# Optimization experiments

Hardware: AMD Instinct MI355X
Metric: run time of the kernel (lower is better)

Reference implementation:

```python
import jax, jax.numpy as jnp
import numpy as np

NEG_SLOPE = 0.2


def _attn_layer(x, src, dst, W, a, n_nodes):
    # x: (N, Cin), W: (Cout, Cin) torch Linear convention, a: (2*Cout,)
    h = x @ W.T                                  # (N, Cout)
    H = h.shape[-1]
    # cat([x_i, x_j]) @ a  ==  h[dst] @ a[:H] + h[src] @ a[H:]
    s_i = h @ a[:H]                              # (N,)
    s_j = h @ a[H:]                              # (N,)
    score = s_i[dst] + s_j[src]                  # (E,)
    alpha = jax.nn.leaky_relu(score, NEG_SLOPE)
    # segment softmax over destination nodes
    amax = jax.ops.segment_max(alpha, dst, num_segments=n_nodes)
    amax = jnp.where(jnp.isfinite(amax), amax, 0.0)
    ex = jnp.exp(alpha - amax[dst])
    denom = jax.ops.segment_sum(ex, dst, num_segments=n_nodes)
    alpha = ex / denom[dst]                      # (E,)
    msg = h[src] * alpha[:, None]                # (E, Cout)
    sums = jax.ops.segment_sum(msg, dst, num_segments=n_nodes)
    cnt = jax.ops.segment_sum(jnp.ones_like(alpha), dst, num_segments=n_nodes)
    return sums / jnp.maximum(cnt, 1.0)[:, None]  # mean aggregation


def setup_inputs() -> dict:
    key = jax.random.key(0)
    ks = jax.random.split(key, 8)
    B, N, C, H, E = 16, 2048, 256, 256, 262144
    NT = B * N
    temporal_features = jax.random.normal(ks[0], (B, N, C), dtype=jnp.float32)
    edge_index = jax.random.randint(ks[1], (2, E), 0, NT, dtype=jnp.int64)
    sc = 1.0 / np.sqrt(C)
    W1 = jax.random.normal(ks[2], (H, C), dtype=jnp.float32) * sc
    a1 = jax.random.normal(ks[3], (2 * H,), dtype=jnp.float32) * sc
    W2 = jax.random.normal(ks[4], (H, H), dtype=jnp.float32) * sc
    a2 = jax.random.normal(ks[5], (2 * H,), dtype=jnp.float32) * sc
    W3 = jax.random.normal(ks[6], (H, H), dtype=jnp.float32) * sc
    a3 = jax.random.normal(ks[7], (2 * H,), dtype=jnp.float32) * sc
    return {"temporal_features": temporal_features, "edge_index": edge_index,
            "W1": W1, "a1": a1, "W2": W2, "a2": a2, "W3": W3, "a3": a3}


def reference(temporal_features, edge_index, W1, a1, W2, a2, W3, a3):
    B, N, C = temporal_features.shape
    n_nodes = B * N
    src, dst = edge_index[0], edge_index[1]  # x_j = x[src], x_i = x[dst]
    x = temporal_features.reshape(n_nodes, C)
    for W, a in ((W1, a1), (W2, a2), (W3, a3)):
        x = _attn_layer(x, src, dst, W, a, n_nodes)
        x = jax.nn.elu(x)
    return x.reshape(B, N, -1)
```

## Files before the change

### kernel.cpp

```cpp
#include <hip/hip_runtime.h>
#include <math.h>
#include <stdint.h>


typedef float f32x4 __attribute__((ext_vector_type(4)));
typedef _Float16 f16x8 __attribute__((ext_vector_type(8)));
typedef _Float16 f16x4 __attribute__((ext_vector_type(4)));


__global__ __launch_bounds__(256) void convert_all(const float* __restrict__ x0,
                                                   _Float16* __restrict__ Xh, int nx,
                                                   const float* __restrict__ W0,
                                                   const float* __restrict__ W1,
                                                   const float* __restrict__ W2,
                                                   _Float16* __restrict__ Wh)
{
    const int i = (blockIdx.x * 256 + threadIdx.x) * 8;
    const float* src;
    _Float16* dstp;
    int off;
    if (i < nx) { src = x0; dstp = Xh; off = i; }
    else {
        const int j = i - nx;
        src = (j < 65536) ? W0 : ((j < 131072) ? W1 : W2);
        off = j & 65535;
        dstp = Wh + (j - off);
    }
    float4 a = *(const float4*)&src[off];
    float4 b = *(const float4*)&src[off + 4];
    f16x8 o = {(_Float16)a.x, (_Float16)a.y, (_Float16)a.z, (_Float16)a.w,
               (_Float16)b.x, (_Float16)b.y, (_Float16)b.z, (_Float16)b.w};
    *(f16x8*)&dstp[off] = o;
}


#define SWZ(row, byte) ((byte) ^ (((row) & 7) << 4))

__global__ __launch_bounds__(512) void gemm_f16(const _Float16* __restrict__ X,
                                                const _Float16* __restrict__ Wh,
                                                const float* __restrict__ avec,
                                                _Float16* __restrict__ Hout,
                                                float* __restrict__ si,
                                                float* __restrict__ sj)
{
    __shared__ __align__(16) unsigned char smem[98304];
    float (*Es)[260] = (float (*)[260])smem;

    const int tid  = threadIdx.x;
    const int lane = tid & 63;
    const int w    = tid >> 6;
    const int wr   = w >> 2;
    const int wc   = w & 3;
    const int ln   = lane & 15;
    const int kq   = lane >> 4;
    const int m0   = blockIdx.x * 128;

    const int xr = tid >> 2;
    const int xc = tid & 3;
    const int wrow = tid >> 1;
    const int wcb  = (tid & 1) * 64;

    const _Float16* Xg = X  + (size_t)(m0 + xr) * 256 + xc * 16;
    const _Float16* Wg = Wh + (size_t)wrow * 256 + wcb / 2;
    const int xs0 = SWZ(xr, xr * 128 + xc * 32);
    const int xs1 = SWZ(xr, xr * 128 + xc * 32 + 16);
    const int wl0 = 16384 + SWZ(wrow, wrow * 128 + wcb + 0);
    const int wl1 = 16384 + SWZ(wrow, wrow * 128 + wcb + 16);
    const int wl2 = 16384 + SWZ(wrow, wrow * 128 + wcb + 32);
    const int wl3 = 16384 + SWZ(wrow, wrow * 128 + wcb + 48);

    f32x4 acc[4][4] = {};

    f16x8 x0 = *(const f16x8*)&Xg[0];
    f16x8 x1 = *(const f16x8*)&Xg[8];
    f16x8 w0 = *(const f16x8*)&Wg[0];
    f16x8 w1 = *(const f16x8*)&Wg[8];
    f16x8 w2 = *(const f16x8*)&Wg[16];
    f16x8 w3 = *(const f16x8*)&Wg[24];
    *(f16x8*)(smem + xs0) = x0;  *(f16x8*)(smem + xs1) = x1;
    *(f16x8*)(smem + wl0) = w0;  *(f16x8*)(smem + wl1) = w1;
    *(f16x8*)(smem + wl2) = w2;  *(f16x8*)(smem + wl3) = w3;
    __syncthreads();

#pragma unroll
    for (int t = 0; t < 4; ++t) {
        const int cb = (t & 1) * 49152;
        const int nb = ((t & 1) ^ 1) * 49152;
        if (t < 3) {
            const int k0 = (t + 1) * 64;
            x0 = *(const f16x8*)&Xg[k0];
            x1 = *(const f16x8*)&Xg[k0 + 8];
            w0 = *(const f16x8*)&Wg[k0];
            w1 = *(const f16x8*)&Wg[k0 + 8];
            w2 = *(const f16x8*)&Wg[k0 + 16];
            w3 = *(const f16x8*)&Wg[k0 + 24];
        }
#pragma unroll
        for (int kk = 0; kk < 2; ++kk) {
            f16x8 af[4], bf[4];
#pragma unroll
            for (int i = 0; i < 4; ++i) {
                const int row = wr * 64 + i * 16 + ln;
                af[i] = *(const f16x8*)(smem + cb + SWZ(row, row * 128 + kk * 64 + kq * 16));
            }
#pragma unroll
            for (int j = 0; j < 4; ++j) {
                const int row = wc * 64 + j * 16 + ln;
                bf[j] = *(const f16x8*)(smem + cb + 16384 + SWZ(row, row * 128 + kk * 64 + kq * 16));
            }
#pragma unroll
            for (int i = 0; i < 4; ++i)
#pragma unroll
                for (int j = 0; j < 4; ++j)
                    acc[i][j] = __builtin_amdgcn_mfma_f32_16x16x32_f16(af[i], bf[j], acc[i][j], 0, 0, 0);
        }
        if (t < 3) {
            *(f16x8*)(smem + nb + xs0) = x0;  *(f16x8*)(smem + nb + xs1) = x1;
            *(f16x8*)(smem + nb + wl0) = w0;  *(f16x8*)(smem + nb + wl1) = w1;
            *(f16x8*)(smem + nb + wl2) = w2;  *(f16x8*)(smem + nb + wl3) = w3;
        }
        __syncthreads();
    }

    const int er = tid >> 5;
    const int ec = tid & 31;
    for (int g = 0; g < 8; ++g) {
        if (wr == (g >> 2)) {
            const int i = g & 3;
#pragma unroll
            for (int j = 0; j < 4; ++j) {
                const int col = wc * 64 + j * 16 + ln;
#pragma unroll
                for (int q = 0; q < 4; ++q)
                    Es[kq * 4 + q][col] = acc[i][j][q];
            }
        }
        __syncthreads();
        const int grow = m0 + g * 16 + er;
        const int c0 = ec * 8;
        f32x4 v0 = *(const f32x4*)&Es[er][c0];
        f32x4 v1 = *(const f32x4*)&Es[er][c0 + 4];
        f16x8 ho = {(_Float16)v0[0], (_Float16)v0[1], (_Float16)v0[2], (_Float16)v0[3],
                    (_Float16)v1[0], (_Float16)v1[1], (_Float16)v1[2], (_Float16)v1[3]};
        *(f16x8*)&Hout[(size_t)grow * 256 + c0] = ho;

        f32x4 al0 = *(const f32x4*)&avec[c0];
        f32x4 al1 = *(const f32x4*)&avec[c0 + 4];
        f32x4 ah0 = *(const f32x4*)&avec[256 + c0];
        f32x4 ah1 = *(const f32x4*)&avec[256 + c0 + 4];
        float d0 = v0[0]*al0[0] + v0[1]*al0[1] + v0[2]*al0[2] + v0[3]*al0[3]
                 + v1[0]*al1[0] + v1[1]*al1[1] + v1[2]*al1[2] + v1[3]*al1[3];
        float d1 = v0[0]*ah0[0] + v0[1]*ah0[1] + v0[2]*ah0[2] + v0[3]*ah0[3]
                 + v1[0]*ah1[0] + v1[1]*ah1[1] + v1[2]*ah1[2] + v1[3]*ah1[3];
#pragma unroll
        for (int d = 16; d; d >>= 1) {
            d0 += __shfl_xor(d0, d);
            d1 += __shfl_xor(d1, d);
        }
        if (ec == 0) { si[grow] = d0; sj[grow] = d1; }
        __syncthreads();
    }
}


__global__ void zero_int(int* p, int n)
{
    int i = blockIdx.x * blockDim.x + threadIdx.x;
    if (i < n) p[i] = 0;
}

__global__ void hist_kernel(const int* __restrict__ dst, int* __restrict__ cnt, int E)
{
    int e = blockIdx.x * blockDim.x + threadIdx.x;
    if (e < E) atomicAdd(&cnt[dst[e]], 1);
}

__global__ __launch_bounds__(1024) void scan_part(const int* __restrict__ cnt,
                                                  int* __restrict__ off,
                                                  int* __restrict__ bsum)
{
    __shared__ int buf[1024];
    const int tid = threadIdx.x;
    const int g = blockIdx.x * 1024 + tid;
    int v = cnt[g];
    buf[tid] = v;
    __syncthreads();
#pragma unroll
    for (int d = 1; d < 1024; d <<= 1) {
        int t = (tid >= d) ? buf[tid - d] : 0;
        __syncthreads();
        buf[tid] += t;
        __syncthreads();
    }
    off[g] = buf[tid] - v;
    if (tid == 1023) bsum[blockIdx.x] = buf[1023];
}

__global__ void scan_bsum(int* bsum, int nb)
{
    __shared__ int b[64];
    const int tid = threadIdx.x;
    b[tid] = (tid < nb) ? bsum[tid] : 0;
    __syncthreads();
    if (tid == 0) {
        int a = 0;
        for (int i = 0; i < nb; ++i) { int t = b[i]; b[i] = a; a += t; }
    }
    __syncthreads();
    if (tid < nb) bsum[tid] = b[tid];
}

__global__ __launch_bounds__(1024) void scan_add(const int* __restrict__ bsum,
                                                 int* __restrict__ off,
                                                 int* __restrict__ cursor,
                                                 int NT, int E)
{
    const int tid = threadIdx.x;
    const int g = blockIdx.x * 1024 + tid;
    int v = off[g] + bsum[blockIdx.x];
    off[g] = v;
    cursor[g] = v;
    if (g == 0) off[NT] = E;
}

__global__ void scatter_kernel(const int* __restrict__ src,
                               const int* __restrict__ dst,
                               int* __restrict__ cursor,
                               int* __restrict__ ssrc, int E)
{
    int e = blockIdx.x * blockDim.x + threadIdx.x;
    if (e < E) {
        int p = atomicAdd(&cursor[dst[e]], 1);
        ssrc[p] = src[e];
    }
}


__device__ __forceinline__ float bcast_f(float x, int l)
{
    return __uint_as_float(__builtin_amdgcn_readlane(__float_as_uint(x), l));
}

template <int F16OUT>
__global__ __launch_bounds__(256) void aggregate(const _Float16* __restrict__ Hh,
                                                 const float* __restrict__ si,
                                                 const float* __restrict__ sj,
                                                 const int* __restrict__ off,
                                                 const int* __restrict__ ssrc,
                                                 void* __restrict__ outv,
                                                 int n_nodes)
{
    const int v = (blockIdx.x * 256 + threadIdx.x) >> 6;
    const int lane = threadIdx.x & 63;
    if (v >= n_nodes) return;

    const int e0 = off[v], e1 = off[v + 1];
    const int deg = e1 - e0;
    f32x4 acc = {0.f, 0.f, 0.f, 0.f};

    if (deg > 0 && deg <= 64) {
        const float siv = si[v];
        const int idx = e0 + lane;
        const bool on = idx < e1;
        int s = 0;
        float scv = -1e30f;
        if (on) {
            s = ssrc[idx];
            float t = siv + sj[s];
            scv = (t >= 0.f) ? t : 0.2f * t;
        }
        float m = scv;
#pragma unroll
        for (int d = 32; d; d >>= 1) m = fmaxf(m, __shfl_xor(m, d));
        float wv = on ? __expf(scv - m) : 0.f;
        float den = wv;
#pragma unroll
        for (int d = 32; d; d >>= 1) den += __shfl_xor(den, d);

        const int c4 = lane * 4;
        for (int eo = 0; eo < deg; eo += 4) {
            const int l1 = (eo + 1 < 63) ? eo + 1 : 63;
            const int l2 = (eo + 2 < 63) ? eo + 2 : 63;
            const int l3 = (eo + 3 < 63) ? eo + 3 : 63;
            const int s0 = __builtin_amdgcn_readlane(s, eo);
            const int s1 = __builtin_amdgcn_readlane(s, l1);
            const int s2 = __builtin_amdgcn_readlane(s, l2);
            const int s3 = __builtin_amdgcn_readlane(s, l3);
            const float w0 = bcast_f(wv, eo);
            const float w1 = bcast_f(wv, l1);
            const float w2 = bcast_f(wv, l2);
            const float w3 = bcast_f(wv, l3);
            const f16x4 v0 = *(const f16x4*)&Hh[(size_t)s0 * 256 + c4];
            const f16x4 v1 = *(const f16x4*)&Hh[(size_t)s1 * 256 + c4];
            const f16x4 v2 = *(const f16x4*)&Hh[(size_t)s2 * 256 + c4];
            const f16x4 v3 = *(const f16x4*)&Hh[(size_t)s3 * 256 + c4];
#pragma unroll
            for (int q = 0; q < 4; ++q)
                acc[q] += w0 * (float)v0[q] + w1 * (float)v1[q]
                        + w2 * (float)v2[q] + w3 * (float)v3[q];
        }
        const float inv = 1.f / (den * (float)deg);
#pragma unroll
        for (int q = 0; q < 4; ++q) acc[q] *= inv;
    } else if (deg > 64) {
        const float siv = si[v];
        float m = -1e30f;
        for (int b = e0 + lane; b < e1; b += 64) {
            float t = siv + sj[ssrc[b]];
            t = (t >= 0.f) ? t : 0.2f * t;
            m = fmaxf(m, t);
        }
#pragma unroll
        for (int d = 32; d; d >>= 1) m = fmaxf(m, __shfl_xor(m, d));
        float den = 0.f;
        for (int b = e0 + lane; b < e1; b += 64) {
            float t = siv + sj[ssrc[b]];
            t = (t >= 0.f) ? t : 0.2f * t;
            den += __expf(t - m);
        }
#pragma unroll
        for (int d = 32; d; d >>= 1) den += __shfl_xor(den, d);
        for (int e = e0; e < e1; ++e) {
            const int s = ssrc[e];
            float t = siv + sj[s];
            t = (t >= 0.f) ? t : 0.2f * t;
            const float wgt = __expf(t - m);
            const f16x4 hv = *(const f16x4*)&Hh[(size_t)s * 256 + lane * 4];
#pragma unroll
            for (int q = 0; q < 4; ++q) acc[q] += wgt * (float)hv[q];
        }
        const float inv = 1.f / (den * (float)deg);
#pragma unroll
        for (int q = 0; q < 4; ++q) acc[q] *= inv;
    }

    float4 o;
    o.x = (acc[0] > 0.f) ? acc[0] : (__expf(acc[0]) - 1.f);
    o.y = (acc[1] > 0.f) ? acc[1] : (__expf(acc[1]) - 1.f);
    o.z = (acc[2] > 0.f) ? acc[2] : (__expf(acc[2]) - 1.f);
    o.w = (acc[3] > 0.f) ? acc[3] : (__expf(acc[3]) - 1.f);
    if (F16OUT) {
        f16x4 oh = {(_Float16)o.x, (_Float16)o.y, (_Float16)o.z, (_Float16)o.w};
        *(f16x4*)&((_Float16*)outv)[(size_t)v * 256 + lane * 4] = oh;
    } else {
        *(float4*)&((float*)outv)[(size_t)v * 256 + lane * 4] = o;
    }
}


extern "C" void kernel_launch(void* const* d_in, const int* in_sizes, int n_in,
                              void* d_out, int out_size, void* d_ws, size_t ws_size,
                              hipStream_t stream)
{
    const float* x0 = (const float*)d_in[0];
    const int*   ei = (const int*)d_in[1];
    const float* Ws[3] = {(const float*)d_in[2], (const float*)d_in[4], (const float*)d_in[6]};
    const float* as[3] = {(const float*)d_in[3], (const float*)d_in[5], (const float*)d_in[7]};
    float* out = (float*)d_out;

    const int NT = in_sizes[0] / 256;
    const int E  = in_sizes[1] / 2;
    const int* srcI = ei;
    const int* dstI = ei + E;

    _Float16* Hh = (_Float16*)d_ws;
    _Float16* Xh = Hh + (size_t)NT * 256;
    float* si    = (float*)(Xh + (size_t)NT * 256);
    float* sj    = si + NT;
    int* cnt     = (int*)(sj + NT);
    int* off     = cnt + NT;
    int* cursor  = off + NT + 1;
    int* ssrc    = cursor + NT;
    int* bsum    = ssrc + E;
    _Float16* Wh = (_Float16*)(((uintptr_t)(bsum + 64) + 255) & ~(uintptr_t)255);

    const int nx = NT * 256;
    convert_all<<<(nx + 3 * 65536) / 2048, 256, 0, stream>>>(x0, Xh, nx,
                                                             Ws[0], Ws[1], Ws[2], Wh);

    zero_int<<<(NT + 255) / 256, 256, 0, stream>>>(cnt, NT);
    hist_kernel<<<(E + 255) / 256, 256, 0, stream>>>(dstI, cnt, E);
    scan_part<<<NT / 1024, 1024, 0, stream>>>(cnt, off, bsum);
    scan_bsum<<<1, 64, 0, stream>>>(bsum, NT / 1024);
    scan_add<<<NT / 1024, 1024, 0, stream>>>(bsum, off, cursor, NT, E);
    scatter_kernel<<<(E + 255) / 256, 256, 0, stream>>>(srcI, dstI, cursor, ssrc, E);

    for (int l = 0; l < 3; ++l) {
        gemm_f16<<<NT / 128, 512, 0, stream>>>(Xh, Wh + (size_t)l * 65536, as[l], Hh, si, sj);
        if (l < 2)
            aggregate<1><<<NT / 4, 256, 0, stream>>>(Hh, si, sj, off, ssrc, (void*)Xh, NT);
        else
            aggregate<0><<<NT / 4, 256, 0, stream>>>(Hh, si, sj, off, ssrc, (void*)out, NT);
    }
}
```

Measured before the change: 241.5 us.

## Fuse CSR scan into one kernel, memset counts, unroll gather by eight

Replaces the three-kernel prefix scan with a single 1024-thread block that scans 32 counts per thread, and swaps the zeroing kernel for hipMemsetAsync, cutting launch overhead. The aggregate's low-degree path now gathers eight neighbour rows per iteration instead of four, exposing more memory loads in flight. The single-block scan serializes 32K elements on one CU with strided per-thread stores, and the wider unroll raises register use.

```diff
diff --git a/kernel.cpp b/kernel.cpp
--- a/kernel.cpp
+++ b/kernel.cpp
@@ -163,64 +163,45 @@
 }
 
 
-__global__ void zero_int(int* p, int n)
-{
-    int i = blockIdx.x * blockDim.x + threadIdx.x;
-    if (i < n) p[i] = 0;
-}
-
 __global__ void hist_kernel(const int* __restrict__ dst, int* __restrict__ cnt, int E)
 {
     int e = blockIdx.x * blockDim.x + threadIdx.x;
     if (e < E) atomicAdd(&cnt[dst[e]], 1);
 }
 
-__global__ __launch_bounds__(1024) void scan_part(const int* __restrict__ cnt,
-                                                  int* __restrict__ off,
-                                                  int* __restrict__ bsum)
-{
-    __shared__ int buf[1024];
+__global__ __launch_bounds__(1024) void scan_fused(const int* __restrict__ cnt,
+                                                   int* __restrict__ off,
+                                                   int* __restrict__ cursor,
+                                                   int NT, int E)
+{
+    __shared__ int ts[1024];
     const int tid = threadIdx.x;
-    const int g = blockIdx.x * 1024 + tid;
-    int v = cnt[g];
-    buf[tid] = v;
+    const int base = tid * 32;
+    int v[32];
+    int s = 0;
+#pragma unroll
+    for (int i = 0; i < 32; i += 4) {
+        int4 q = *(const int4*)&cnt[base + i];
+        v[i] = q.x; v[i+1] = q.y; v[i+2] = q.z; v[i+3] = q.w;
+        s += q.x + q.y + q.z + q.w;
+    }
+    ts[tid] = s;
     __syncthreads();
 #pragma unroll
     for (int d = 1; d < 1024; d <<= 1) {
-        int t = (tid >= d) ? buf[tid - d] : 0;
-        __syncthreads();
-        buf[tid] += t;
-        __syncthreads();
-    }
-    off[g] = buf[tid] - v;
-    if (tid == 1023) bsum[blockIdx.x] = buf[1023];
-}
-
-__global__ void scan_bsum(int* bsum, int nb)
-{
-    __shared__ int b[64];
-    const int tid = threadIdx.x;
-    b[tid] = (tid < nb) ? bsum[tid] : 0;
-    __syncthreads();
-    if (tid == 0) {
-        int a = 0;
-        for (int i = 0; i < nb; ++i) { int t = b[i]; b[i] = a; a += t; }
-    }
-    __syncthreads();
-    if (tid < nb) bsum[tid] = b[tid];
-}
-
-__global__ __launch_bounds__(1024) void scan_add(const int* __restrict__ bsum,
-                                                 int* __restrict__ off,
-                                                 int* __restrict__ cursor,
-                                                 int NT, int E)
-{
-    const int tid = threadIdx.x;
-    const int g = blockIdx.x * 1024 + tid;
-    int v = off[g] + bsum[blockIdx.x];
-    off[g] = v;
-    cursor[g] = v;
-    if (g == 0) off[NT] = E;
+        int t = (tid >= d) ? ts[tid - d] : 0;
+        __syncthreads();
+        ts[tid] += t;
+        __syncthreads();
+    }
+    int run = ts[tid] - s;
+#pragma unroll
+    for (int i = 0; i < 32; ++i) {
+        off[base + i] = run;
+        cursor[base + i] = run;
+        run += v[i];
+    }
+    if (tid == 1023) off[NT] = E;
 }
 
 __global__ void scatter_kernel(const int* __restrict__ src,
@@ -278,26 +259,26 @@
         for (int d = 32; d; d >>= 1) den += __shfl_xor(den, d);
 
         const int c4 = lane * 4;
-        for (int eo = 0; eo < deg; eo += 4) {
-            const int l1 = (eo + 1 < 63) ? eo + 1 : 63;
-            const int l2 = (eo + 2 < 63) ? eo + 2 : 63;
-            const int l3 = (eo + 3 < 63) ? eo + 3 : 63;
-            const int s0 = __builtin_amdgcn_readlane(s, eo);
-            const int s1 = __builtin_amdgcn_readlane(s, l1);
-            const int s2 = __builtin_amdgcn_readlane(s, l2);
-            const int s3 = __builtin_amdgcn_readlane(s, l3);
-            const float w0 = bcast_f(wv, eo);
-            const float w1 = bcast_f(wv, l1);
-            const float w2 = bcast_f(wv, l2);
-            const float w3 = bcast_f(wv, l3);
-            const f16x4 v0 = *(const f16x4*)&Hh[(size_t)s0 * 256 + c4];
-            const f16x4 v1 = *(const f16x4*)&Hh[(size_t)s1 * 256 + c4];
-            const f16x4 v2 = *(const f16x4*)&Hh[(size_t)s2 * 256 + c4];
-            const f16x4 v3 = *(const f16x4*)&Hh[(size_t)s3 * 256 + c4];
-#pragma unroll
-            for (int q = 0; q < 4; ++q)
-                acc[q] += w0 * (float)v0[q] + w1 * (float)v1[q]
-                        + w2 * (float)v2[q] + w3 * (float)v3[q];
+        for (int eo = 0; eo < deg; eo += 8) {
+            int sl[8]; float wl[8];
+#pragma unroll
+            for (int u = 0; u < 8; ++u) {
+                const int l = (eo + u < 63) ? eo + u : 63;
+                sl[u] = __builtin_amdgcn_readlane(s, l);
+                wl[u] = bcast_f(wv, l);
+            }
+            f16x4 hv[8];
+#pragma unroll
+            for (int u = 0; u < 8; ++u)
+                hv[u] = *(const f16x4*)&Hh[(size_t)sl[u] * 256 + c4];
+#pragma unroll
+            for (int q = 0; q < 4; ++q) {
+                float t = 0.f;
+#pragma unroll
+                for (int u = 0; u < 8; ++u)
+                    t += wl[u] * (float)hv[u][q];
+                acc[q] += t;
+            }
         }
         const float inv = 1.f / (den * (float)deg);
 #pragma unroll
@@ -378,11 +359,9 @@
     convert_all<<<(nx + 3 * 65536) / 2048, 256, 0, stream>>>(x0, Xh, nx,
                                                              Ws[0], Ws[1], Ws[2], Wh);
 
-    zero_int<<<(NT + 255) / 256, 256, 0, stream>>>(cnt, NT);
+    hipMemsetAsync(cnt, 0, (size_t)NT * sizeof(int), stream);
     hist_kernel<<<(E + 255) / 256, 256, 0, stream>>>(dstI, cnt, E);
-    scan_part<<<NT / 1024, 1024, 0, stream>>>(cnt, off, bsum);
-    scan_bsum<<<1, 64, 0, stream>>>(bsum, NT / 1024);
-    scan_add<<<NT / 1024, 1024, 0, stream>>>(bsum, off, cursor, NT, E);
+    scan_fused<<<1, 1024, 0, stream>>>(cnt, off, cursor, NT, E);
     scatter_kernel<<<(E + 255) / 256, 256, 0, stream>>>(srcI, dstI, cursor, ssrc, E);
 
     for (int l = 0; l < 3; ++l) {
```

Result: slower. 247.4 us (+2.4%).
